# Optimization experiments

Measured on AMD Instinct MI355X. Metric: run time of the kernel, lower is better.

Reference implementation:

```python
import jax, jax.numpy as jnp
import numpy as np

LOW_DIM, SKIP_DIM, OUT_DIM = 512, 256, 256
EPS_IDW = 1e-8
EPS_LN = 1e-5
K = 3


def setup_inputs() -> dict:
    key = jax.random.key(0)
    ks = jax.random.split(key, 10)
    B, N, S = 4, 8192, 2048
    xyz_hi = jax.random.uniform(ks[0], (B, N, 3), dtype=jnp.float32)
    xyz_lo = jax.random.uniform(ks[1], (B, S, 3), dtype=jnp.float32)
    feat_skip = jax.random.normal(ks[2], (B, N, SKIP_DIM), dtype=jnp.float32)
    feat_lo = jax.random.normal(ks[3], (B, S, LOW_DIM), dtype=jnp.float32)
    in_dim = LOW_DIM + SKIP_DIM
    W1 = jax.random.normal(ks[4], (in_dim, OUT_DIM), dtype=jnp.float32) / np.sqrt(in_dim)
    b1 = jnp.zeros((OUT_DIM,), dtype=jnp.float32)
    W2 = jax.random.normal(ks[5], (OUT_DIM, OUT_DIM), dtype=jnp.float32) / np.sqrt(OUT_DIM)
    b2 = jnp.zeros((OUT_DIM,), dtype=jnp.float32)
    gamma = jnp.ones((OUT_DIM,), dtype=jnp.float32)
    beta = jnp.zeros((OUT_DIM,), dtype=jnp.float32)
    return {"xyz_hi": xyz_hi, "xyz_lo": xyz_lo, "feat_skip": feat_skip,
            "feat_lo": feat_lo, "W1": W1, "b1": b1, "W2": W2, "b2": b2,
            "gamma": gamma, "beta": beta}


def _layer_norm(x, gamma, beta):
    mu = jnp.mean(x, axis=-1, keepdims=True)
    var = jnp.mean(jnp.square(x - mu), axis=-1, keepdims=True)
    return (x - mu) * jax.lax.rsqrt(var + EPS_LN) * gamma + beta


def reference(xyz_hi, xyz_lo, feat_skip, feat_lo, W1, b1, W2, b2, gamma, beta):
    B, N, _ = xyz_hi.shape
    _, S, _ = xyz_lo.shape
    if S == 1:
        interpolated = jnp.broadcast_to(feat_lo, (B, N, feat_lo.shape[-1]))
    else:
        # pairwise Euclidean distances: (B, N, S)
        d2 = (jnp.sum(xyz_hi ** 2, -1)[:, :, None]
              + jnp.sum(xyz_lo ** 2, -1)[:, None, :]
              - 2.0 * jnp.einsum('bnd,bsd->bns', xyz_hi, xyz_lo))
        dists = jnp.sqrt(jnp.maximum(d2, 0.0))
        # smallest-3 via top_k on negated distances
        neg_d, knn_idx = jax.lax.top_k(-dists, K)          # (B, N, 3)
        dk = -neg_d
        inv_d = 1.0 / (dk + EPS_IDW)
        weights = inv_d / jnp.sum(inv_d, axis=-1, keepdims=True)  # (B, N, 3)
        # gather neighbor features: (B, N, 3, low_dim)
        knn_feat = feat_lo[jnp.arange(B)[:, None, None], knn_idx]
        interpolated = jnp.einsum('bnk,bnkc->bnc', weights, knn_feat)
    fused = jnp.concatenate([feat_skip, interpolated], axis=-1)   # (B, N, skip+low)
    h = jax.nn.relu(fused @ W1 + b1)
    h = h @ W2 + b2
    return _layer_norm(h, gamma, beta)
```

## Files before the change

kernel.cpp:

```cpp
#include <hip/hip_runtime.h>
#include <hip/hip_bf16.h>
#include <stdint.h>

typedef unsigned short u16;
typedef __attribute__((ext_vector_type(8))) short short8;
typedef __attribute__((ext_vector_type(4))) float f32x4;

#define BB 4
#define NN 8192
#define SS 2048
#define MTOT 32768
#define CSKIP 256
#define CLO 512
#define CIN 768
#define COUT 256

__device__ __forceinline__ u16 f2bf(float f) {
  unsigned u = __float_as_uint(f);
  u += 0x7fffu + ((u >> 16) & 1u);
  return (u16)(u >> 16);
}

__device__ __forceinline__ void gl_lds16(const void* g, void* l) {
  __builtin_amdgcn_global_load_lds(
      (const __attribute__((address_space(1))) void*)g,
      (__attribute__((address_space(3))) void*)l, 16, 0, 0);
}

__global__ __launch_bounds__(1024) void knn_wconv_kernel(
    const float* __restrict__ xyz_hi, const float* __restrict__ xyz_lo,
    const float* __restrict__ W1, const float* __restrict__ W2,
    float* __restrict__ wq_g, int* __restrict__ iq_g,
    u16* __restrict__ W1aT, u16* __restrict__ W1bT, u16* __restrict__ W2T) {
  int blk = blockIdx.x;
  int tid = threadIdx.x;
  if (blk >= 512) {
    int base = (blk - 512) * 1024 + tid;
    for (int i = base; i < 262144; i += 65536) {
      if (i < 65536) {
        int n = i >> 8, k = i & 255;
        W1aT[i] = f2bf(W1[(size_t)k * COUT + n]);
      } else if (i < 196608) {
        int j = i - 65536;
        int n = j >> 9, k = j & 511;
        W1bT[j] = f2bf(W1[(size_t)(256 + k) * COUT + n]);
      } else {
        int j = i - 196608;
        int n = j >> 8, k = j & 255;
        W2T[j] = f2bf(W2[(size_t)k * COUT + n]);
      }
    }
    return;
  }

  __shared__ float md[16][64][3];
  __shared__ int   mi[16][64][3];

  int b = blk >> 7;
  int wave = tid >> 6, lane = tid & 63;
  int qm = blk * 64 + lane;
  float qx = xyz_hi[(size_t)qm * 3 + 0];
  float qy = xyz_hi[(size_t)qm * 3 + 1];
  float qz = xyz_hi[(size_t)qm * 3 + 2];

  const float* xl = xyz_lo + (size_t)b * SS * 3;
  int j0 = __builtin_amdgcn_readfirstlane(wave * 128);

  float b0 = 1e30f, b1 = 1e30f, b2 = 1e30f;
  int i0 = -1, i1 = -1, i2 = -1;
#pragma unroll 8
  for (int jj = 0; jj < 128; ++jj) {
    int j = j0 + jj;
    float px = xl[3 * j + 0];
    float py = xl[3 * j + 1];
    float pz = xl[3 * j + 2];
    float dx = px - qx, dy = py - qy, dz = pz - qz;
    float d = fmaf(dx, dx, fmaf(dy, dy, dz * dz));
    bool c0 = d < b0, c1 = d < b1, c2 = d < b2;
    float nb0 = fminf(b0, d);
    float nb1 = __builtin_amdgcn_fmed3f(b0, b1, d);
    float nb2 = __builtin_amdgcn_fmed3f(b1, b2, d);
    int ni0 = c0 ? j : i0;
    int ni1 = c0 ? i0 : (c1 ? j : i1);
    int ni2 = c1 ? i1 : (c2 ? j : i2);
    b0 = nb0; b1 = nb1; b2 = nb2;
    i0 = ni0; i1 = ni1; i2 = ni2;
  }
  md[wave][lane][0] = b0; mi[wave][lane][0] = i0;
  md[wave][lane][1] = b1; mi[wave][lane][1] = i1;
  md[wave][lane][2] = b2; mi[wave][lane][2] = i2;
  __syncthreads();

  if (tid < 64) {
    int q = tid;
    float fb0 = 1e30f, fb1 = 1e30f, fb2 = 1e30f;
    int fi0 = -1, fi1 = -1, fi2 = -1;
    for (int p = 0; p < 16; ++p)
#pragma unroll
      for (int s = 0; s < 3; ++s) {
        float d = md[p][q][s]; int ix = mi[p][q][s];
        if (d < fb2 || (d == fb2 && ix < fi2)) {
          fb2 = d; fi2 = ix;
          if (fb2 < fb1 || (fb2 == fb1 && fi2 < fi1)) {
            float t = fb1; fb1 = fb2; fb2 = t; int ti = fi1; fi1 = fi2; fi2 = ti;
          }
          if (fb1 < fb0 || (fb1 == fb0 && fi1 < fi0)) {
            float t = fb0; fb0 = fb1; fb1 = t; int ti = fi0; fi0 = fi1; fi1 = ti;
          }
        }
      }
    int qm2 = blk * 64 + q;
    float d0 = sqrtf(fb0), d1 = sqrtf(fb1), d2 = sqrtf(fb2);
    float inv0 = 1.0f / (d0 + 1e-8f);
    float inv1 = 1.0f / (d1 + 1e-8f);
    float inv2 = 1.0f / (d2 + 1e-8f);
    float s = inv0 + inv1 + inv2;
    wq_g[(size_t)qm2 * 3 + 0] = inv0 / s;
    wq_g[(size_t)qm2 * 3 + 1] = inv1 / s;
    wq_g[(size_t)qm2 * 3 + 2] = inv2 / s;
    iq_g[(size_t)qm2 * 3 + 0] = fi0;
    iq_g[(size_t)qm2 * 3 + 1] = fi1;
    iq_g[(size_t)qm2 * 3 + 2] = fi2;
  }
}

__global__ __launch_bounds__(256, 4) void ggemm_kernel(
    const float* __restrict__ feat_lo, const u16* __restrict__ W1bT,
    float* __restrict__ G) {
  __shared__ u16 As[32 * 40];
  __shared__ u16 Bs[128 * 32];
  int tid = threadIdx.x;
  int m0 = (blockIdx.x >> 1) << 5;
  int n0 = (blockIdx.x & 1) << 7;
  int w = tid >> 6, lane = tid & 63;
  int quad = lane >> 4, l16 = lane & 15;

  int srow = tid >> 3, s4 = (tid & 7) << 2;
  const float* arow = feat_lo + (size_t)(m0 + srow) * CLO + s4;
  u16* As_dst = As + srow * 40 + s4;

  f32x4 zero = {0.f, 0.f, 0.f, 0.f};
  f32x4 acc[2][2];
#pragma unroll
  for (int tm = 0; tm < 2; ++tm)
#pragma unroll
    for (int tn = 0; tn < 2; ++tn) acc[tm][tn] = zero;

  for (int kc = 0; kc < 16; ++kc) {
    __syncthreads();
#pragma unroll
    for (int r = 0; r < 2; ++r) {
      int u = tid + r * 256;
      int nrow = u >> 2, c = u & 3;
      int cg = c ^ (nrow & 3);
      gl_lds16(W1bT + (size_t)(n0 + nrow) * CLO + kc * 32 + cg * 8,
               (char*)Bs + u * 16);
    }
    float4 av = *(const float4*)(arow + kc * 32);
    union { __hip_bfloat162 h2[2]; uint2 u2; } pk;
    pk.h2[0] = __float22bfloat162_rn(make_float2(av.x, av.y));
    pk.h2[1] = __float22bfloat162_rn(make_float2(av.z, av.w));
    *(uint2*)As_dst = pk.u2;
    __syncthreads();

    short8 af[2], bf[2];
#pragma unroll
    for (int t = 0; t < 2; ++t)
      af[t] = *(const short8*)(As + (t * 16 + l16) * 40 + quad * 8);
#pragma unroll
    for (int t = 0; t < 2; ++t) {
      int rr = w * 32 + t * 16 + l16;
      bf[t] = *(const short8*)(Bs + (rr * 4 + (quad ^ (rr & 3))) * 8);
    }
#pragma unroll
    for (int tm = 0; tm < 2; ++tm)
#pragma unroll
      for (int tn = 0; tn < 2; ++tn)
        acc[tm][tn] = __builtin_amdgcn_mfma_f32_16x16x32_bf16(af[tm], bf[tn], acc[tm][tn], 0, 0, 0);
  }

#pragma unroll
  for (int tm = 0; tm < 2; ++tm)
#pragma unroll
    for (int tn = 0; tn < 2; ++tn) {
      int col = n0 + w * 32 + tn * 16 + l16;
#pragma unroll
      for (int r = 0; r < 4; ++r) {
        int row = m0 + tm * 16 + quad * 4 + r;
        G[(size_t)row * COUT + col] = acc[tm][tn][r];
      }
    }
}

__global__ __launch_bounds__(256, 4) void gemm12_kernel(
    const float* __restrict__ feat_skip, const u16* __restrict__ W1aT,
    const float* __restrict__ b1, const float* __restrict__ G,
    const float* __restrict__ wq_g, const int* __restrict__ iq_g,
    const u16* __restrict__ W2T, const float* __restrict__ b2,
    const float* __restrict__ gamma, const float* __restrict__ beta,
    float* __restrict__ out) {
  __shared__ u16 Hs[32 * 264];
  __shared__ u16 Bs[256 * 32];
  __shared__ u16 As[32 * 40];
  __shared__ float swq[96];
  __shared__ int   siq[96];
  __shared__ float red[4][32][2];
  __shared__ float stats[32][2];
  int tid = threadIdx.x;
  int m0 = blockIdx.x << 5;
  int bS = (m0 >> 13) * SS;
  int w = tid >> 6, lane = tid & 63;
  int quad = lane >> 4, l16 = lane & 15;

  if (tid < 96) {
    swq[tid] = wq_g[(size_t)m0 * 3 + tid];
    siq[tid] = iq_g[(size_t)m0 * 3 + tid];
  }

  int srow = tid >> 3, sc4 = (tid & 7) << 2;
  const float* arow = feat_skip + (size_t)(m0 + srow) * CSKIP + sc4;
  u16* As_dst = As + srow * 40 + sc4;

  f32x4 zero = {0.f, 0.f, 0.f, 0.f};
  f32x4 acc[2][4];
#pragma unroll
  for (int tm = 0; tm < 2; ++tm)
#pragma unroll
    for (int tn = 0; tn < 4; ++tn) acc[tm][tn] = zero;

  for (int kc = 0; kc < 8; ++kc) {
    __syncthreads();
#pragma unroll
    for (int r = 0; r < 4; ++r) {
      int u = tid + r * 256;
      int nrow = u >> 2, c = u & 3;
      int cg = c ^ (nrow & 3);
      gl_lds16(W1aT + (size_t)nrow * CSKIP + kc * 32 + cg * 8, (char*)Bs + u * 16);
    }
    float4 av = *(const float4*)(arow + kc * 32);
    union { __hip_bfloat162 h2[2]; uint2 u2; } pk;
    pk.h2[0] = __float22bfloat162_rn(make_float2(av.x, av.y));
    pk.h2[1] = __float22bfloat162_rn(make_float2(av.z, av.w));
    *(uint2*)As_dst = pk.u2;
    __syncthreads();

    short8 af[2], bf[4];
#pragma unroll
    for (int t = 0; t < 2; ++t)
      af[t] = *(const short8*)(As + (t * 16 + l16) * 40 + quad * 8);
#pragma unroll
    for (int t = 0; t < 4; ++t) {
      int rr = w * 64 + t * 16 + l16;
      bf[t] = *(const short8*)(Bs + (rr * 4 + (quad ^ (rr & 3))) * 8);
    }
#pragma unroll
    for (int tm = 0; tm < 2; ++tm)
#pragma unroll
      for (int tn = 0; tn < 4; ++tn)
        acc[tm][tn] = __builtin_amdgcn_mfma_f32_16x16x32_bf16(af[tm], bf[tn], acc[tm][tn], 0, 0, 0);
  }

  {
    float bias[4];
#pragma unroll
    for (int tn = 0; tn < 4; ++tn) bias[tn] = b1[w * 64 + tn * 16 + l16];
#pragma unroll
    for (int tm = 0; tm < 2; ++tm)
#pragma unroll
      for (int r = 0; r < 4; ++r) {
        int rl = tm * 16 + quad * 4 + r;
        float w0 = swq[rl * 3 + 0], w1 = swq[rl * 3 + 1], w2 = swq[rl * 3 + 2];
        const float* g0 = G + (size_t)(bS + siq[rl * 3 + 0]) * COUT;
        const float* g1 = G + (size_t)(bS + siq[rl * 3 + 1]) * COUT;
        const float* g2 = G + (size_t)(bS + siq[rl * 3 + 2]) * COUT;
#pragma unroll
        for (int tn = 0; tn < 4; ++tn) {
          int col = w * 64 + tn * 16 + l16;
          float gv = fmaf(w0, g0[col], fmaf(w1, g1[col], w2 * g2[col]));
          float v = acc[tm][tn][r] + bias[tn] + gv;
          v = v > 0.f ? v : 0.f;
          Hs[rl * 264 + col] = f2bf(v);
        }
      }
  }

#pragma unroll
  for (int tm = 0; tm < 2; ++tm)
#pragma unroll
    for (int tn = 0; tn < 4; ++tn) acc[tm][tn] = zero;

  for (int kc = 0; kc < 8; ++kc) {
    __syncthreads();
#pragma unroll
    for (int r = 0; r < 4; ++r) {
      int u = tid + r * 256;
      int nrow = u >> 2, c = u & 3;
      int cg = c ^ (nrow & 3);
      gl_lds16(W2T + (size_t)nrow * COUT + kc * 32 + cg * 8, (char*)Bs + u * 16);
    }
    __syncthreads();

    short8 af[2], bf[4];
#pragma unroll
    for (int t = 0; t < 2; ++t)
      af[t] = *(const short8*)(Hs + (t * 16 + l16) * 264 + kc * 32 + quad * 8);
#pragma unroll
    for (int t = 0; t < 4; ++t) {
      int rr = w * 64 + t * 16 + l16;
      bf[t] = *(const short8*)(Bs + (rr * 4 + (quad ^ (rr & 3))) * 8);
    }
#pragma unroll
    for (int tm = 0; tm < 2; ++tm)
#pragma unroll
      for (int tn = 0; tn < 4; ++tn)
        acc[tm][tn] = __builtin_amdgcn_mfma_f32_16x16x32_bf16(af[tm], bf[tn], acc[tm][tn], 0, 0, 0);
  }

  float bias[4], g[4], be[4];
#pragma unroll
  for (int tn = 0; tn < 4; ++tn) {
    int col = w * 64 + tn * 16 + l16;
    bias[tn] = b2[col]; g[tn] = gamma[col]; be[tn] = beta[col];
  }
#pragma unroll
  for (int tm = 0; tm < 2; ++tm)
#pragma unroll
    for (int r = 0; r < 4; ++r) {
      float s = 0.f, sq = 0.f;
#pragma unroll
      for (int tn = 0; tn < 4; ++tn) {
        float v = acc[tm][tn][r] + bias[tn];
        acc[tm][tn][r] = v;
        s += v; sq += v * v;
      }
#pragma unroll
      for (int msk = 1; msk < 16; msk <<= 1) {
        s += __shfl_xor(s, msk);
        sq += __shfl_xor(sq, msk);
      }
      if (l16 == 0) {
        int rl = tm * 16 + quad * 4 + r;
        red[w][rl][0] = s;
        red[w][rl][1] = sq;
      }
    }
  __syncthreads();
  if (tid < 32) {
    float s = red[0][tid][0] + red[1][tid][0] + red[2][tid][0] + red[3][tid][0];
    float sq = red[0][tid][1] + red[1][tid][1] + red[2][tid][1] + red[3][tid][1];
    float mu = s * (1.f / 256.f);
    float var = sq * (1.f / 256.f) - mu * mu;
    stats[tid][0] = mu;
    stats[tid][1] = rsqrtf(var + 1e-5f);
  }
  __syncthreads();
#pragma unroll
  for (int tm = 0; tm < 2; ++tm)
#pragma unroll
    for (int r = 0; r < 4; ++r) {
      int rl = tm * 16 + quad * 4 + r;
      float mu = stats[rl][0], rstd = stats[rl][1];
#pragma unroll
      for (int tn = 0; tn < 4; ++tn) {
        int col = w * 64 + tn * 16 + l16;
        out[(size_t)(m0 + rl) * COUT + col] = (acc[tm][tn][r] - mu) * rstd * g[tn] + be[tn];
      }
    }
}

extern "C" void kernel_launch(void* const* d_in, const int* in_sizes, int n_in,
                              void* d_out, int out_size, void* d_ws, size_t ws_size,
                              hipStream_t stream) {
  const float* xyz_hi    = (const float*)d_in[0];
  const float* xyz_lo    = (const float*)d_in[1];
  const float* feat_skip = (const float*)d_in[2];
  const float* feat_lo   = (const float*)d_in[3];
  const float* W1        = (const float*)d_in[4];
  const float* b1        = (const float*)d_in[5];
  const float* W2        = (const float*)d_in[6];
  const float* b2        = (const float*)d_in[7];
  const float* gamma     = (const float*)d_in[8];
  const float* beta      = (const float*)d_in[9];
  float* out = (float*)d_out;

  char* ws = (char*)d_ws;
  u16*   W1aT  = (u16*)(ws + 16777216);
  u16*   W1bT  = (u16*)(ws + 16908288);
  u16*   W2T   = (u16*)(ws + 17170432);
  float* wq_g  = (float*)(ws + 17301504);
  int*   iq_g  = (int*)(ws + 17694720);
  float* G     = (float*)(ws + 18087936);

  knn_wconv_kernel<<<576, 1024, 0, stream>>>(xyz_hi, xyz_lo, W1, W2,
                                             wq_g, iq_g, W1aT, W1bT, W2T);
  ggemm_kernel<<<(BB * SS) / 32 * 2, 256, 0, stream>>>(feat_lo, W1bT, G);
  gemm12_kernel<<<MTOT / 32, 256, 0, stream>>>(feat_skip, W1aT, b1, G, wq_g, iq_g,
                                               W2T, b2, gamma, beta, out);
}
```

Before: 186.6 us.

## Load MFMA fragments directly from global memory, dropping LDS staging in GEMMs

Both GEMM kernels stop staging A and B tiles through LDS with global_load_lds and per-chunk barriers. Each lane now loads its MFMA fragments straight from global memory, converting feat_lo and feat_skip to bf16 in registers, and the K loops are fully unrolled. The goal is to remove barrier stalls and LDS traffic and to raise occupancy (ggemm launch bound raised to 6). The cost is duplicated global and L2 reads of each operand across waves, plus 32-byte strided row accesses that coalesce worse.

```diff
diff --git a/kernel.cpp b/kernel.cpp
--- a/kernel.cpp
+++ b/kernel.cpp
@@ -21,10 +21,15 @@
   return (u16)(u >> 16);
 }
 
-__device__ __forceinline__ void gl_lds16(const void* g, void* l) {
-  __builtin_amdgcn_global_load_lds(
-      (const __attribute__((address_space(1))) void*)g,
-      (__attribute__((address_space(3))) void*)l, 16, 0, 0);
+__device__ __forceinline__ short8 pack_bf8(const float* p) {
+  float4 x0 = *(const float4*)(p);
+  float4 x1 = *(const float4*)(p + 4);
+  union { __hip_bfloat162 h2[4]; short8 s8; } pk;
+  pk.h2[0] = __float22bfloat162_rn(make_float2(x0.x, x0.y));
+  pk.h2[1] = __float22bfloat162_rn(make_float2(x0.z, x0.w));
+  pk.h2[2] = __float22bfloat162_rn(make_float2(x1.x, x1.y));
+  pk.h2[3] = __float22bfloat162_rn(make_float2(x1.z, x1.w));
+  return pk.s8;
 }
 
 __global__ __launch_bounds__(1024) void knn_wconv_kernel(
@@ -124,21 +129,15 @@
   }
 }
 
-__global__ __launch_bounds__(256, 4) void ggemm_kernel(
+__global__ __launch_bounds__(256, 6) void ggemm_kernel(
     const float* __restrict__ feat_lo, const u16* __restrict__ W1bT,
     float* __restrict__ G) {
-  __shared__ u16 As[32 * 40];
-  __shared__ u16 Bs[128 * 32];
   int tid = threadIdx.x;
   int m0 = (blockIdx.x >> 1) << 5;
   int n0 = (blockIdx.x & 1) << 7;
   int w = tid >> 6, lane = tid & 63;
   int quad = lane >> 4, l16 = lane & 15;
 
-  int srow = tid >> 3, s4 = (tid & 7) << 2;
-  const float* arow = feat_lo + (size_t)(m0 + srow) * CLO + s4;
-  u16* As_dst = As + srow * 40 + s4;
-
   f32x4 zero = {0.f, 0.f, 0.f, 0.f};
   f32x4 acc[2][2];
 #pragma unroll
@@ -146,32 +145,18 @@
 #pragma unroll
     for (int tn = 0; tn < 2; ++tn) acc[tm][tn] = zero;
 
+  const float* a0p = feat_lo + (size_t)(m0 + l16) * CLO + quad * 8;
+  const float* a1p = a0p + 16 * CLO;
+  const u16* b0p = W1bT + (size_t)(n0 + w * 32 + l16) * CLO + quad * 8;
+  const u16* b1p = b0p + 16 * CLO;
+
+#pragma unroll
   for (int kc = 0; kc < 16; ++kc) {
-    __syncthreads();
-#pragma unroll
-    for (int r = 0; r < 2; ++r) {
-      int u = tid + r * 256;
-      int nrow = u >> 2, c = u & 3;
-      int cg = c ^ (nrow & 3);
-      gl_lds16(W1bT + (size_t)(n0 + nrow) * CLO + kc * 32 + cg * 8,
-               (char*)Bs + u * 16);
-    }
-    float4 av = *(const float4*)(arow + kc * 32);
-    union { __hip_bfloat162 h2[2]; uint2 u2; } pk;
-    pk.h2[0] = __float22bfloat162_rn(make_float2(av.x, av.y));
-    pk.h2[1] = __float22bfloat162_rn(make_float2(av.z, av.w));
-    *(uint2*)As_dst = pk.u2;
-    __syncthreads();
-
     short8 af[2], bf[2];
-#pragma unroll
-    for (int t = 0; t < 2; ++t)
-      af[t] = *(const short8*)(As + (t * 16 + l16) * 40 + quad * 8);
-#pragma unroll
-    for (int t = 0; t < 2; ++t) {
-      int rr = w * 32 + t * 16 + l16;
-      bf[t] = *(const short8*)(Bs + (rr * 4 + (quad ^ (rr & 3))) * 8);
-    }
+    af[0] = pack_bf8(a0p + kc * 32);
+    af[1] = pack_bf8(a1p + kc * 32);
+    bf[0] = *(const short8*)(b0p + kc * 32);
+    bf[1] = *(const short8*)(b1p + kc * 32);
 #pragma unroll
     for (int tm = 0; tm < 2; ++tm)
 #pragma unroll
@@ -200,8 +185,6 @@
     const float* __restrict__ gamma, const float* __restrict__ beta,
     float* __restrict__ out) {
   __shared__ u16 Hs[32 * 264];
-  __shared__ u16 Bs[256 * 32];
-  __shared__ u16 As[32 * 40];
   __shared__ float swq[96];
   __shared__ int   siq[96];
   __shared__ float red[4][32][2];
@@ -217,10 +200,6 @@
     siq[tid] = iq_g[(size_t)m0 * 3 + tid];
   }
 
-  int srow = tid >> 3, sc4 = (tid & 7) << 2;
-  const float* arow = feat_skip + (size_t)(m0 + srow) * CSKIP + sc4;
-  u16* As_dst = As + srow * 40 + sc4;
-
   f32x4 zero = {0.f, 0.f, 0.f, 0.f};
   f32x4 acc[2][4];
 #pragma unroll
@@ -228,37 +207,30 @@
 #pragma unroll
     for (int tn = 0; tn < 4; ++tn) acc[tm][tn] = zero;
 
-  for (int kc = 0; kc < 8; ++kc) {
-    __syncthreads();
-#pragma unroll
-    for (int r = 0; r < 4; ++r) {
-      int u = tid + r * 256;
-      int nrow = u >> 2, c = u & 3;
-      int cg = c ^ (nrow & 3);
-      gl_lds16(W1aT + (size_t)nrow * CSKIP + kc * 32 + cg * 8, (char*)Bs + u * 16);
-    }
-    float4 av = *(const float4*)(arow + kc * 32);
-    union { __hip_bfloat162 h2[2]; uint2 u2; } pk;
-    pk.h2[0] = __float22bfloat162_rn(make_float2(av.x, av.y));
-    pk.h2[1] = __float22bfloat162_rn(make_float2(av.z, av.w));
-    *(uint2*)As_dst = pk.u2;
-    __syncthreads();
-
-    short8 af[2], bf[4];
-#pragma unroll
-    for (int t = 0; t < 2; ++t)
-      af[t] = *(const short8*)(As + (t * 16 + l16) * 40 + quad * 8);
-#pragma unroll
-    for (int t = 0; t < 4; ++t) {
-      int rr = w * 64 + t * 16 + l16;
-      bf[t] = *(const short8*)(Bs + (rr * 4 + (quad ^ (rr & 3))) * 8);
-    }
-#pragma unroll
-    for (int tm = 0; tm < 2; ++tm)
-#pragma unroll
-      for (int tn = 0; tn < 4; ++tn)
-        acc[tm][tn] = __builtin_amdgcn_mfma_f32_16x16x32_bf16(af[tm], bf[tn], acc[tm][tn], 0, 0, 0);
-  }
+  {
+    const float* a0p = feat_skip + (size_t)(m0 + l16) * CSKIP + quad * 8;
+    const float* a1p = a0p + 16 * CSKIP;
+    const u16* bp[4];
+#pragma unroll
+    for (int t = 0; t < 4; ++t)
+      bp[t] = W1aT + (size_t)(w * 64 + t * 16 + l16) * CSKIP + quad * 8;
+
+#pragma unroll
+    for (int kc = 0; kc < 8; ++kc) {
+      short8 af[2], bf[4];
+      af[0] = pack_bf8(a0p + kc * 32);
+      af[1] = pack_bf8(a1p + kc * 32);
+#pragma unroll
+      for (int t = 0; t < 4; ++t) bf[t] = *(const short8*)(bp[t] + kc * 32);
+#pragma unroll
+      for (int tm = 0; tm < 2; ++tm)
+#pragma unroll
+        for (int tn = 0; tn < 4; ++tn)
+          acc[tm][tn] = __builtin_amdgcn_mfma_f32_16x16x32_bf16(af[tm], bf[tn], acc[tm][tn], 0, 0, 0);
+    }
+  }
+
+  __syncthreads();
 
   {
     float bias[4];
@@ -284,36 +256,33 @@
       }
   }
 
+  __syncthreads();
+
 #pragma unroll
   for (int tm = 0; tm < 2; ++tm)
 #pragma unroll
     for (int tn = 0; tn < 4; ++tn) acc[tm][tn] = zero;
 
-  for (int kc = 0; kc < 8; ++kc) {
-    __syncthreads();
-#pragma unroll
-    for (int r = 0; r < 4; ++r) {
-      int u = tid + r * 256;
-      int nrow = u >> 2, c = u & 3;
-      int cg = c ^ (nrow & 3);
-      gl_lds16(W2T + (size_t)nrow * COUT + kc * 32 + cg * 8, (char*)Bs + u * 16);
-    }
-    __syncthreads();
-
-    short8 af[2], bf[4];
-#pragma unroll
-    for (int t = 0; t < 2; ++t)
-      af[t] = *(const short8*)(Hs + (t * 16 + l16) * 264 + kc * 32 + quad * 8);
-#pragma unroll
-    for (int t = 0; t < 4; ++t) {
-      int rr = w * 64 + t * 16 + l16;
-      bf[t] = *(const short8*)(Bs + (rr * 4 + (quad ^ (rr & 3))) * 8);
-    }
-#pragma unroll
-    for (int tm = 0; tm < 2; ++tm)
-#pragma unroll
-      for (int tn = 0; tn < 4; ++tn)
-        acc[tm][tn] = __builtin_amdgcn_mfma_f32_16x16x32_bf16(af[tm], bf[tn], acc[tm][tn], 0, 0, 0);
+  {
+    const u16* bp[4];
+#pragma unroll
+    for (int t = 0; t < 4; ++t)
+      bp[t] = W2T + (size_t)(w * 64 + t * 16 + l16) * COUT + quad * 8;
+
+#pragma unroll
+    for (int kc = 0; kc < 8; ++kc) {
+      short8 af[2], bf[4];
+#pragma unroll
+      for (int t = 0; t < 2; ++t)
+        af[t] = *(const short8*)(Hs + (t * 16 + l16) * 264 + kc * 32 + quad * 8);
+#pragma unroll
+      for (int t = 0; t < 4; ++t) bf[t] = *(const short8*)(bp[t] + kc * 32);
+#pragma unroll
+      for (int tm = 0; tm < 2; ++tm)
+#pragma unroll
+        for (int tn = 0; tn < 4; ++tn)
+          acc[tm][tn] = __builtin_amdgcn_mfma_f32_16x16x32_bf16(af[tm], bf[tn], acc[tm][tn], 0, 0, 0);
+    }
   }
 
   float bias[4], g[4], be[4];
```

Result: slower. 212.3 us (+13.8%).
